# Kernel optimization log

Hardware: AMD Instinct MI355X
Metric: run time of the kernel (lower is better)

Reference implementation:

```python
import jax, jax.numpy as jnp
import numpy as np

B, S, HIDDEN = 8, 2048, 1024
NUM_GROUPS, NUM_VARS = 2, 320
CODEVECTOR_DIM = 256
TAU = 2.0  # module hardcodes self.temperature = 2
EPS_U = 1e-6


def setup_inputs() -> dict:
    key = jax.random.key(0)
    k1, k2, k3, k4 = jax.random.split(key, 4)
    hidden_states = jax.random.normal(k1, (B, S, HIDDEN), dtype=jnp.float32)
    W = jax.random.normal(k2, (NUM_GROUPS * NUM_VARS, HIDDEN), dtype=jnp.float32) * 0.02
    b = jnp.zeros((NUM_GROUPS * NUM_VARS,), dtype=jnp.float32)
    codevectors = jax.random.normal(
        k3, (1, NUM_GROUPS * NUM_VARS, CODEVECTOR_DIM // NUM_GROUPS), dtype=jnp.float32)
    gumbel_u = jax.random.uniform(
        k4, (B * S * NUM_GROUPS, NUM_VARS), minval=EPS_U, maxval=1.0 - EPS_U, dtype=jnp.float32)
    return {"hidden_states": hidden_states, "W": W, "b": b,
            "codevectors": codevectors, "gumbel_u": gumbel_u}


def reference(hidden_states, W, b, codevectors, gumbel_u):
    Bs, Ss, H = hidden_states.shape
    G, V = NUM_GROUPS, NUM_VARS
    N = Bs * Ss
    # weight_proj: [B,S,H] -> [B,S,G*V]
    logits = jnp.einsum('bsh,vh->bsv', hidden_states, W) + b
    logits = logits.reshape(N * G, V)
    # gumbel_softmax(tau=2, hard=True) -- training path
    gumbel = -jnp.log(-jnp.log(gumbel_u))
    y_soft = jax.nn.softmax((logits + gumbel) / TAU, axis=-1)
    idx = jnp.argmax(y_soft, axis=-1)
    y_hard = jax.nn.one_hot(idx, V, dtype=y_soft.dtype)
    # straight-through (hard value, soft gradient)
    codevector_probs = y_hard + y_soft - jax.lax.stop_gradient(y_soft)
    # perplexity over the soft (non-gumbel) distribution
    soft_dist = jax.nn.softmax(logits.reshape(N, G, V), axis=-1)
    marginal = soft_dist.mean(axis=0)                      # [G, V]
    perplexity = jnp.exp(-jnp.sum(marginal * jnp.log(marginal + 1e-7), axis=-1)).sum()
    # one-hot probs x codevectors, grouped sum: [N,G,V] x [G,V,d] -> [N,G,d]
    cv = codevectors.reshape(G, V, CODEVECTOR_DIM // G)
    out = jnp.einsum('ngv,gvd->ngd', codevector_probs.reshape(N, G, V), cv)
    out = out.reshape(Bs, Ss, CODEVECTOR_DIM)
    return out, perplexity
```

## Files before the change

### kernel.cpp

```cpp
#include <hip/hip_runtime.h>
#include <math.h>

#define NROWS 16384
#define HIDDEN 1024
#define NGROUPS 2
#define NVARS 320
#define NCOLS 640
#define CVDIM 256
#define OUT_ELEMS (NROWS * CVDIM)

#define BM 64
#define BK 32
#define NTHREADS 512
#define LGS 324

typedef __attribute__((ext_vector_type(8))) short short8;
typedef __attribute__((ext_vector_type(4))) float floatx4;

__device__ __forceinline__ ushort f32_to_bf16(float f) {
    unsigned u = __builtin_bit_cast(unsigned, f);
    unsigned r = (u + 0x7FFFu + ((u >> 16) & 1u)) >> 16;
    return (ushort)r;
}
__device__ __forceinline__ float bf16_to_f32(ushort u) {
    return __builtin_bit_cast(float, ((unsigned)u) << 16);
}

__global__ __launch_bounds__(256) void convert_bf16_kernel(
    const float* __restrict__ src, ushort* __restrict__ dst, int n8)
{
    const int i = blockIdx.x * 256 + threadIdx.x;
    if (i >= n8) return;
    const float4* s = reinterpret_cast<const float4*>(src) + (size_t)i * 2;
    const float4 v0 = s[0];
    const float4 v1 = s[1];
    uint4 p;
    p.x = (unsigned)f32_to_bf16(v0.x) | ((unsigned)f32_to_bf16(v0.y) << 16);
    p.y = (unsigned)f32_to_bf16(v0.z) | ((unsigned)f32_to_bf16(v0.w) << 16);
    p.z = (unsigned)f32_to_bf16(v1.x) | ((unsigned)f32_to_bf16(v1.y) << 16);
    p.w = (unsigned)f32_to_bf16(v1.z) | ((unsigned)f32_to_bf16(v1.w) << 16);
    reinterpret_cast<uint4*>(dst)[i] = p;
}

__device__ __forceinline__ void async16(const ushort* g, ushort* l) {
    __builtin_amdgcn_global_load_lds(
        (const __attribute__((address_space(1))) void*)g,
        (__attribute__((address_space(3))) void*)l,
        16, 0, 0);
}

__global__ __launch_bounds__(NTHREADS, 4) void fused_gvq_kernel(
    const float* __restrict__ X,
    const ushort* __restrict__ Wbf,
    const float* __restrict__ bias,
    const float* __restrict__ gu,
    const float* __restrict__ cv,
    float* __restrict__ out,
    float* __restrict__ marginal)
{
    __shared__ __align__(16) ushort lds[64 * LGS];
    ushort* As = lds;
    ushort* Bs = lds + 2048;

    const int tid = threadIdx.x;
    const int lane = tid & 63;
    const int w = tid >> 6;
    const int wm = w >> 2;
    const int wn = w & 3;
    const int mtile = blockIdx.x >> 1;
    const int g = blockIdx.x & 1;
    const int m0 = mtile * BM;
    const int n0 = g * NVARS;

    const int rm = lane & 15;
    const int kc = lane >> 4;

    floatx4 acc[2][5];
#pragma unroll
    for (int i = 0; i < 2; ++i)
#pragma unroll
        for (int j = 0; j < 5; ++j) acc[i][j] = (floatx4){0.f, 0.f, 0.f, 0.f};

    const int arow = tid >> 3;
    const int ak4 = (tid & 7) * 4;
    const float* Abase = X + (size_t)(m0 + arow) * HIDDEN + ak4;
    float4 areg = *reinterpret_cast<const float4*>(Abase);

    for (int k0 = 0; k0 < HIDDEN; k0 += BK) {
        uint2 pk;
        pk.x = (unsigned)f32_to_bf16(areg.x) | ((unsigned)f32_to_bf16(areg.y) << 16);
        pk.y = (unsigned)f32_to_bf16(areg.z) | ((unsigned)f32_to_bf16(areg.w) << 16);
        *reinterpret_cast<uint2*>(&As[arow * 32 + ak4]) = pk;
        {
            int c = tid;
            async16(Wbf + (size_t)(n0 + (c >> 2)) * HIDDEN + k0 + (c & 3) * 8, Bs + c * 8);
            c = tid + 512;
            async16(Wbf + (size_t)(n0 + (c >> 2)) * HIDDEN + k0 + (c & 3) * 8, Bs + c * 8);
            if (tid < 256) {
                c = tid + 1024;
                async16(Wbf + (size_t)(n0 + (c >> 2)) * HIDDEN + k0 + (c & 3) * 8, Bs + c * 8);
            }
        }
        __syncthreads();

        if (k0 + BK < HIDDEN)
            areg = *reinterpret_cast<const float4*>(Abase + k0 + BK);

        const short8* Asv = reinterpret_cast<const short8*>(As);
        const short8* Bsv = reinterpret_cast<const short8*>(Bs);
        short8 af[2], bf[5];
#pragma unroll
        for (int i = 0; i < 2; ++i)
            af[i] = Asv[(wm * 32 + i * 16 + rm) * 4 + kc];
#pragma unroll
        for (int j = 0; j < 5; ++j)
            bf[j] = Bsv[(wn * 80 + j * 16 + rm) * 4 + kc];
#pragma unroll
        for (int i = 0; i < 2; ++i)
#pragma unroll
            for (int j = 0; j < 5; ++j)
                acc[i][j] = __builtin_amdgcn_mfma_f32_16x16x32_bf16(
                    af[i], bf[j], acc[i][j], 0, 0, 0);
        __syncthreads();
    }

    const int cl = lane & 15;
    const int r4 = (lane >> 4) * 4;

    {
        float bj[5];
#pragma unroll
        for (int j = 0; j < 5; ++j) bj[j] = bias[n0 + wn * 80 + j * 16 + cl];
#pragma unroll
        for (int i = 0; i < 2; ++i)
#pragma unroll
            for (int j = 0; j < 5; ++j) {
                const int col = wn * 80 + j * 16 + cl;
#pragma unroll
                for (int q = 0; q < 4; ++q) {
                    const int lrow = wm * 32 + i * 16 + r4 + q;
                    lds[lrow * LGS + col] = f32_to_bf16(acc[i][j][q] + bj[j]);
                }
            }
    }
    __syncthreads();

    float macc[5];
#pragma unroll
    for (int j = 0; j < 5; ++j) macc[j] = 0.f;

    for (int s = 0; s < 8; ++s) {
        const int lrow = s * 8 + w;
        const int n = m0 + lrow;
        const size_t goff = ((size_t)n * 2 + g) * NVARS;

        float u5[5], lg[5];
#pragma unroll
        for (int j = 0; j < 5; ++j) u5[j] = gu[goff + lane + j * 64];
#pragma unroll
        for (int j = 0; j < 5; ++j) lg[j] = bf16_to_f32(lds[lrow * LGS + lane + j * 64]);

        float bk = lg[0] - __logf(-__logf(u5[0]));
        int bi = lane;
#pragma unroll
        for (int j = 1; j < 5; ++j) {
            const float kj = lg[j] - __logf(-__logf(u5[j]));
            const int v = lane + j * 64;
            if (kj > bk) { bk = kj; bi = v; }
        }
#pragma unroll
        for (int sh = 32; sh > 0; sh >>= 1) {
            const float ok = __shfl_xor(bk, sh);
            const int oi = __shfl_xor(bi, sh);
            if (ok > bk || (ok == bk && oi < bi)) { bk = ok; bi = oi; }
        }

        float p[5], sume = 0.f;
#pragma unroll
        for (int j = 0; j < 5; ++j) { p[j] = __expf(lg[j]); sume += p[j]; }
#pragma unroll
        for (int sh = 32; sh > 0; sh >>= 1) sume += __shfl_xor(sume, sh);
        const float inv = 1.f / sume;
#pragma unroll
        for (int j = 0; j < 5; ++j) macc[j] += p[j] * inv;

        const float2* cvrow =
            reinterpret_cast<const float2*>(cv + (size_t)(n0 + bi) * 128);
        reinterpret_cast<float2*>(out + (size_t)n * CVDIM + g * 128)[lane] = cvrow[lane];
    }

    __syncthreads();
    float* smr = reinterpret_cast<float*>(lds);
#pragma unroll
    for (int j = 0; j < 5; ++j) smr[w * NVARS + lane + j * 64] = macc[j];
    __syncthreads();
    if (tid < NVARS) {
        float sm = 0.f;
#pragma unroll
        for (int ww = 0; ww < 8; ++ww) sm += smr[ww * NVARS + tid];
        atomicAdd(&marginal[n0 + tid], sm);
    }
}

__global__ void perplexity_kernel(const float* __restrict__ marginal,
                                  float* __restrict__ out)
{
    const int lane = threadIdx.x;
    float h0 = 0.0f, h1 = 0.0f;
    for (int v = lane; v < NVARS; v += 64) {
        const float m0 = marginal[v] * (1.0f / (float)NROWS);
        h0 += m0 * logf(m0 + 1e-7f);
        const float m1 = marginal[NVARS + v] * (1.0f / (float)NROWS);
        h1 += m1 * logf(m1 + 1e-7f);
    }
#pragma unroll
    for (int s = 32; s > 0; s >>= 1) {
        h0 += __shfl_xor(h0, s);
        h1 += __shfl_xor(h1, s);
    }
    if (lane == 0) out[OUT_ELEMS] = expf(-h0) + expf(-h1);
}

extern "C" void kernel_launch(void* const* d_in, const int* in_sizes, int n_in,
                              void* d_out, int out_size, void* d_ws, size_t ws_size,
                              hipStream_t stream) {
    const float* X    = (const float*)d_in[0];
    const float* W    = (const float*)d_in[1];
    const float* bias = (const float*)d_in[2];
    const float* cv   = (const float*)d_in[3];
    const float* gu   = (const float*)d_in[4];
    float* out = (float*)d_out;

    ushort* Wbf      = (ushort*)d_ws;
    float*  marginal = (float*)(Wbf + (size_t)NCOLS * HIDDEN);

    hipMemsetAsync(marginal, 0, NCOLS * sizeof(float), stream);

    convert_bf16_kernel<<<(NCOLS * HIDDEN / 8 + 255) / 256, 256, 0, stream>>>(
        W, Wbf, NCOLS * HIDDEN / 8);

    fused_gvq_kernel<<<(NROWS / BM) * 2, NTHREADS, 0, stream>>>(
        X, Wbf, bias, gu, cv, out, marginal);

    perplexity_kernel<<<1, 64, 0, stream>>>(marginal, out);
}
```

Measured before the change: 69.26 us.

## Double-buffer GEMM LDS tiles and prefetch gumbel noise before epilogue sync

The K-loop now uses two LDS buffers for the A and B tiles. The next tile's bf16 A write and async B load are issued while MFMAs run on the current tile, and global A loads are prefetched two steps ahead. This removes one barrier per iteration and hides load latency behind compute. Gumbel uniforms for all eight epilogue rows are also loaded into registers before the post-GEMM barrier, so their latency overlaps the logits store. The trade is a larger LDS footprint and about 40 extra VGPRs per thread, which could limit occupancy or cause spills.

Measured after the change: 68.72 us. Within noise of the previous version (-0.8%).

```diff
diff --git a/kernel.cpp b/kernel.cpp
--- a/kernel.cpp
+++ b/kernel.cpp
@@ -3,7 +3,6 @@
 
 #define NROWS 16384
 #define HIDDEN 1024
-#define NGROUPS 2
 #define NVARS 320
 #define NCOLS 640
 #define CVDIM 256
@@ -13,14 +12,14 @@
 #define BK 32
 #define NTHREADS 512
 #define LGS 324
+#define BUFS 12288
 
 typedef __attribute__((ext_vector_type(8))) short short8;
 typedef __attribute__((ext_vector_type(4))) float floatx4;
 
-__device__ __forceinline__ ushort f32_to_bf16(float f) {
+__device__ __forceinline__ unsigned f32_to_bf16(float f) {
     unsigned u = __builtin_bit_cast(unsigned, f);
-    unsigned r = (u + 0x7FFFu + ((u >> 16) & 1u)) >> 16;
-    return (ushort)r;
+    return (u + 0x7FFFu + ((u >> 16) & 1u)) >> 16;
 }
 __device__ __forceinline__ float bf16_to_f32(ushort u) {
     return __builtin_bit_cast(float, ((unsigned)u) << 16);
@@ -35,10 +34,10 @@
     const float4 v0 = s[0];
     const float4 v1 = s[1];
     uint4 p;
-    p.x = (unsigned)f32_to_bf16(v0.x) | ((unsigned)f32_to_bf16(v0.y) << 16);
-    p.y = (unsigned)f32_to_bf16(v0.z) | ((unsigned)f32_to_bf16(v0.w) << 16);
-    p.z = (unsigned)f32_to_bf16(v1.x) | ((unsigned)f32_to_bf16(v1.y) << 16);
-    p.w = (unsigned)f32_to_bf16(v1.z) | ((unsigned)f32_to_bf16(v1.w) << 16);
+    p.x = f32_to_bf16(v0.x) | (f32_to_bf16(v0.y) << 16);
+    p.y = f32_to_bf16(v0.z) | (f32_to_bf16(v0.w) << 16);
+    p.z = f32_to_bf16(v1.x) | (f32_to_bf16(v1.y) << 16);
+    p.w = f32_to_bf16(v1.z) | (f32_to_bf16(v1.w) << 16);
     reinterpret_cast<uint4*>(dst)[i] = p;
 }
 
@@ -58,9 +57,7 @@
     float* __restrict__ out,
     float* __restrict__ marginal)
 {
-    __shared__ __align__(16) ushort lds[64 * LGS];
-    ushort* As = lds;
-    ushort* Bs = lds + 2048;
+    __shared__ __align__(16) ushort lds[2 * BUFS];
 
     const int tid = threadIdx.x;
     const int lane = tid & 63;
@@ -84,30 +81,50 @@
     const int arow = tid >> 3;
     const int ak4 = (tid & 7) * 4;
     const float* Abase = X + (size_t)(m0 + arow) * HIDDEN + ak4;
+
+#define WRITE_A(dstAs, v)                                                     \
+    {                                                                         \
+        uint2 pk;                                                             \
+        pk.x = f32_to_bf16((v).x) | (f32_to_bf16((v).y) << 16);               \
+        pk.y = f32_to_bf16((v).z) | (f32_to_bf16((v).w) << 16);               \
+        *reinterpret_cast<uint2*>(&(dstAs)[arow * 32 + ak4]) = pk;            \
+    }
+
+#define ISSUE_B(dstBs, kk)                                                    \
+    {                                                                         \
+        int c = tid;                                                          \
+        async16(Wbf + (size_t)(n0 + (c >> 2)) * HIDDEN + (kk) + (c & 3) * 8,  \
+                (dstBs) + c * 8);                                             \
+        c = tid + 512;                                                        \
+        async16(Wbf + (size_t)(n0 + (c >> 2)) * HIDDEN + (kk) + (c & 3) * 8,  \
+                (dstBs) + c * 8);                                             \
+        if (tid < 256) {                                                      \
+            c = tid + 1024;                                                   \
+            async16(Wbf + (size_t)(n0 + (c >> 2)) * HIDDEN + (kk) + (c & 3) * 8, \
+                    (dstBs) + c * 8);                                         \
+        }                                                                     \
+    }
+
     float4 areg = *reinterpret_cast<const float4*>(Abase);
-
-    for (int k0 = 0; k0 < HIDDEN; k0 += BK) {
-        uint2 pk;
-        pk.x = (unsigned)f32_to_bf16(areg.x) | ((unsigned)f32_to_bf16(areg.y) << 16);
-        pk.y = (unsigned)f32_to_bf16(areg.z) | ((unsigned)f32_to_bf16(areg.w) << 16);
-        *reinterpret_cast<uint2*>(&As[arow * 32 + ak4]) = pk;
-        {
-            int c = tid;
-            async16(Wbf + (size_t)(n0 + (c >> 2)) * HIDDEN + k0 + (c & 3) * 8, Bs + c * 8);
-            c = tid + 512;
-            async16(Wbf + (size_t)(n0 + (c >> 2)) * HIDDEN + k0 + (c & 3) * 8, Bs + c * 8);
-            if (tid < 256) {
-                c = tid + 1024;
-                async16(Wbf + (size_t)(n0 + (c >> 2)) * HIDDEN + k0 + (c & 3) * 8, Bs + c * 8);
-            }
+    WRITE_A(lds, areg);
+    ISSUE_B(lds + 2048, 0);
+    areg = *reinterpret_cast<const float4*>(Abase + BK);
+    __syncthreads();
+
+    for (int t = 0; t < 32; ++t) {
+        const int cur = t & 1;
+        ushort* base_c = lds + cur * BUFS;
+        ushort* base_n = lds + (cur ^ 1) * BUFS;
+
+        if (t < 31) {
+            WRITE_A(base_n, areg);
+            ISSUE_B(base_n + 2048, (t + 1) * BK);
         }
-        __syncthreads();
-
-        if (k0 + BK < HIDDEN)
-            areg = *reinterpret_cast<const float4*>(Abase + k0 + BK);
-
-        const short8* Asv = reinterpret_cast<const short8*>(As);
-        const short8* Bsv = reinterpret_cast<const short8*>(Bs);
+        if (t < 30)
+            areg = *reinterpret_cast<const float4*>(Abase + (t + 2) * BK);
+
+        const short8* Asv = reinterpret_cast<const short8*>(base_c);
+        const short8* Bsv = reinterpret_cast<const short8*>(base_c + 2048);
         short8 af[2], bf[5];
 #pragma unroll
         for (int i = 0; i < 2; ++i)
@@ -139,32 +156,40 @@
 #pragma unroll
                 for (int q = 0; q < 4; ++q) {
                     const int lrow = wm * 32 + i * 16 + r4 + q;
-                    lds[lrow * LGS + col] = f32_to_bf16(acc[i][j][q] + bj[j]);
+                    lds[lrow * LGS + col] = (ushort)f32_to_bf16(acc[i][j][q] + bj[j]);
                 }
             }
     }
+
+    float gup[8][5];
+#pragma unroll
+    for (int s = 0; s < 8; ++s) {
+        const int n = m0 + s * 8 + w;
+        const size_t goff = ((size_t)n * 2 + g) * NVARS + lane;
+#pragma unroll
+        for (int j = 0; j < 5; ++j) gup[s][j] = gu[goff + j * 64];
+    }
     __syncthreads();
 
     float macc[5];
 #pragma unroll
     for (int j = 0; j < 5; ++j) macc[j] = 0.f;
 
+#pragma unroll
     for (int s = 0; s < 8; ++s) {
         const int lrow = s * 8 + w;
         const int n = m0 + lrow;
-        const size_t goff = ((size_t)n * 2 + g) * NVARS;
-
-        float u5[5], lg[5];
-#pragma unroll
-        for (int j = 0; j < 5; ++j) u5[j] = gu[goff + lane + j * 64];
-#pragma unroll
-        for (int j = 0; j < 5; ++j) lg[j] = bf16_to_f32(lds[lrow * LGS + lane + j * 64]);
-
-        float bk = lg[0] - __logf(-__logf(u5[0]));
+
+        float lg[5];
+#pragma unroll
+        for (int j = 0; j < 5; ++j)
+            lg[j] = bf16_to_f32(lds[lrow * LGS + lane + j * 64]);
+
+        float bk = lg[0] - __logf(-__logf(gup[s][0]));
         int bi = lane;
 #pragma unroll
         for (int j = 1; j < 5; ++j) {
-            const float kj = lg[j] - __logf(-__logf(u5[j]));
+            const float kj = lg[j] - __logf(-__logf(gup[s][j]));
             const int v = lane + j * 64;
             if (kj > bk) { bk = kj; bi = v; }
         }
```

## Split fused kernel into tiled double-buffered GEMM and separate quantize pass

Applied to the files above, without the earlier changes.

Splits the fused GEMM+gumbel kernel in two. The first is a 128x128-tile bf16 MFMA GEMM with double-buffered LDS and register prefetch of X, writing bf16 logits to a workspace buffer. The second is a quantize kernel that reads those logits back for argmax, softmax and codevector gather. The goal is to stop each block re-reading X for its group, since the old grid converted X twice, and to improve MFMA reuse and occupancy. The cost is an extra global round-trip of 16384x640 bf16 logits and one more kernel launch.

Measured after the change: 95.44 us. 1.38x slower.

```diff
diff --git a/kernel.cpp b/kernel.cpp
--- a/kernel.cpp
+++ b/kernel.cpp
@@ -3,24 +3,17 @@
 
 #define NROWS 16384
 #define HIDDEN 1024
-#define NGROUPS 2
 #define NVARS 320
 #define NCOLS 640
 #define CVDIM 256
 #define OUT_ELEMS (NROWS * CVDIM)
 
-#define BM 64
-#define BK 32
-#define NTHREADS 512
-#define LGS 324
-
 typedef __attribute__((ext_vector_type(8))) short short8;
 typedef __attribute__((ext_vector_type(4))) float floatx4;
 
-__device__ __forceinline__ ushort f32_to_bf16(float f) {
+__device__ __forceinline__ unsigned f32_to_bf16(float f) {
     unsigned u = __builtin_bit_cast(unsigned, f);
-    unsigned r = (u + 0x7FFFu + ((u >> 16) & 1u)) >> 16;
-    return (ushort)r;
+    return (u + 0x7FFFu + ((u >> 16) & 1u)) >> 16;
 }
 __device__ __forceinline__ float bf16_to_f32(ushort u) {
     return __builtin_bit_cast(float, ((unsigned)u) << 16);
@@ -35,10 +28,10 @@
     const float4 v0 = s[0];
     const float4 v1 = s[1];
     uint4 p;
-    p.x = (unsigned)f32_to_bf16(v0.x) | ((unsigned)f32_to_bf16(v0.y) << 16);
-    p.y = (unsigned)f32_to_bf16(v0.z) | ((unsigned)f32_to_bf16(v0.w) << 16);
-    p.z = (unsigned)f32_to_bf16(v1.x) | ((unsigned)f32_to_bf16(v1.y) << 16);
-    p.w = (unsigned)f32_to_bf16(v1.z) | ((unsigned)f32_to_bf16(v1.w) << 16);
+    p.x = f32_to_bf16(v0.x) | (f32_to_bf16(v0.y) << 16);
+    p.y = f32_to_bf16(v0.z) | (f32_to_bf16(v0.w) << 16);
+    p.z = f32_to_bf16(v1.x) | (f32_to_bf16(v1.y) << 16);
+    p.w = f32_to_bf16(v1.z) | (f32_to_bf16(v1.w) << 16);
     reinterpret_cast<uint4*>(dst)[i] = p;
 }
 
@@ -49,116 +42,154 @@
         16, 0, 0);
 }
 
-__global__ __launch_bounds__(NTHREADS, 4) void fused_gvq_kernel(
+#define GBM 128
+#define GBN 128
+#define GBK 32
+
+__global__ __launch_bounds__(256, 3) void gemm_logits_kernel(
     const float* __restrict__ X,
     const ushort* __restrict__ Wbf,
     const float* __restrict__ bias,
+    ushort* __restrict__ Lg)
+{
+    __shared__ __align__(16) ushort lds[16384];
+
+    const int tid = threadIdx.x;
+    const int lane = tid & 63;
+    const int w = tid >> 6;
+    const int wm = w >> 1, wn = w & 1;
+
+    const int bid = blockIdx.x;
+    const int wg = (bid & 7) * 80 + (bid >> 3);
+    const int m0 = (wg / 5) * GBM;
+    const int n0 = (wg % 5) * GBN;
+
+    const int rm = lane & 15;
+    const int kc = lane >> 4;
+
+    floatx4 acc[4][4];
+#pragma unroll
+    for (int i = 0; i < 4; ++i)
+#pragma unroll
+        for (int j = 0; j < 4; ++j) acc[i][j] = (floatx4){0.f, 0.f, 0.f, 0.f};
+
+    const int arow = tid >> 1;
+    const int acol = (tid & 1) * 16;
+    const float* Aptr = X + (size_t)(m0 + arow) * HIDDEN + acol;
+
+    float4 a0, a1, a2, a3;
+#define LOAD_A(kk) { const float* p = Aptr + (kk);                             \
+    a0 = *(const float4*)(p);      a1 = *(const float4*)(p + 4);               \
+    a2 = *(const float4*)(p + 8);  a3 = *(const float4*)(p + 12); }
+
+#define WRITE_A(dst) { uint4 lo, hi;                                           \
+    lo.x = f32_to_bf16(a0.x) | (f32_to_bf16(a0.y) << 16);                      \
+    lo.y = f32_to_bf16(a0.z) | (f32_to_bf16(a0.w) << 16);                      \
+    lo.z = f32_to_bf16(a1.x) | (f32_to_bf16(a1.y) << 16);                      \
+    lo.w = f32_to_bf16(a1.z) | (f32_to_bf16(a1.w) << 16);                      \
+    hi.x = f32_to_bf16(a2.x) | (f32_to_bf16(a2.y) << 16);                      \
+    hi.y = f32_to_bf16(a2.z) | (f32_to_bf16(a2.w) << 16);                      \
+    hi.z = f32_to_bf16(a3.x) | (f32_to_bf16(a3.y) << 16);                      \
+    hi.w = f32_to_bf16(a3.z) | (f32_to_bf16(a3.w) << 16);                      \
+    uint4* d = (uint4*)((char*)(dst) + arow * 64 + acol * 2);                  \
+    d[0] = lo; d[1] = hi; }
+
+#define ISSUE_B(dst, kk) {                                                     \
+    int c = tid;                                                               \
+    async16(Wbf + (size_t)(n0 + (c >> 2)) * HIDDEN + (kk) + (c & 3) * 8,       \
+            (dst) + c * 8);                                                    \
+    c = tid + 256;                                                             \
+    async16(Wbf + (size_t)(n0 + (c >> 2)) * HIDDEN + (kk) + (c & 3) * 8,       \
+            (dst) + c * 8); }
+
+    LOAD_A(0);
+    WRITE_A(lds);
+    ISSUE_B(lds + 8192, 0);
+    LOAD_A(GBK);
+    __syncthreads();
+
+    for (int t = 0; t < 32; ++t) {
+        const int cur = t & 1;
+        ushort* Ac = lds + (cur ? 4096 : 0);
+        ushort* An = lds + (cur ? 0 : 4096);
+        ushort* Bc = lds + (cur ? 12288 : 8192);
+        ushort* Bn = lds + (cur ? 8192 : 12288);
+        if (t < 31) {
+            WRITE_A(An);
+            ISSUE_B(Bn, (t + 1) * GBK);
+        }
+        if (t < 30) LOAD_A((t + 2) * GBK);
+
+        const short8* Asv = reinterpret_cast<const short8*>(Ac);
+        const short8* Bsv = reinterpret_cast<const short8*>(Bc);
+        short8 af[4], bf[4];
+#pragma unroll
+        for (int f = 0; f < 4; ++f) {
+            af[f] = Asv[(wm * 64 + f * 16 + rm) * 4 + kc];
+            bf[f] = Bsv[(wn * 64 + f * 16 + rm) * 4 + kc];
+        }
+#pragma unroll
+        for (int i = 0; i < 4; ++i)
+#pragma unroll
+            for (int j = 0; j < 4; ++j)
+                acc[i][j] = __builtin_amdgcn_mfma_f32_16x16x32_bf16(
+                    af[i], bf[j], acc[i][j], 0, 0, 0);
+        __syncthreads();
+    }
+
+    const int cl = lane & 15;
+    const int r4 = (lane >> 4) * 4;
+    float bj[4];
+#pragma unroll
+    for (int j = 0; j < 4; ++j) bj[j] = bias[n0 + wn * 64 + j * 16 + cl];
+
+#pragma unroll
+    for (int i = 0; i < 4; ++i)
+#pragma unroll
+        for (int j = 0; j < 4; ++j) {
+            const int col = n0 + wn * 64 + j * 16 + cl;
+#pragma unroll
+            for (int q = 0; q < 4; ++q) {
+                const int row = m0 + wm * 64 + i * 16 + r4 + q;
+                unsigned v = f32_to_bf16(acc[i][j][q] + bj[j]);
+                unsigned o = (unsigned)__shfl_xor((int)v, 1);
+                if ((cl & 1) == 0)
+                    *reinterpret_cast<uint*>(Lg + (size_t)row * NCOLS + col) =
+                        v | (o << 16);
+            }
+        }
+}
+
+__global__ __launch_bounds__(256) void quantize_kernel(
+    const ushort* __restrict__ Lg,
     const float* __restrict__ gu,
     const float* __restrict__ cv,
     float* __restrict__ out,
     float* __restrict__ marginal)
 {
-    __shared__ __align__(16) ushort lds[64 * LGS];
-    ushort* As = lds;
-    ushort* Bs = lds + 2048;
-
+    __shared__ float smr[4][NVARS];
     const int tid = threadIdx.x;
+    const int w = tid >> 6;
     const int lane = tid & 63;
-    const int w = tid >> 6;
-    const int wm = w >> 2;
-    const int wn = w & 3;
-    const int mtile = blockIdx.x >> 1;
-    const int g = blockIdx.x & 1;
-    const int m0 = mtile * BM;
-    const int n0 = g * NVARS;
-
-    const int rm = lane & 15;
-    const int kc = lane >> 4;
-
-    floatx4 acc[2][5];
-#pragma unroll
-    for (int i = 0; i < 2; ++i)
-#pragma unroll
-        for (int j = 0; j < 5; ++j) acc[i][j] = (floatx4){0.f, 0.f, 0.f, 0.f};
-
-    const int arow = tid >> 3;
-    const int ak4 = (tid & 7) * 4;
-    const float* Abase = X + (size_t)(m0 + arow) * HIDDEN + ak4;
-    float4 areg = *reinterpret_cast<const float4*>(Abase);
-
-    for (int k0 = 0; k0 < HIDDEN; k0 += BK) {
-        uint2 pk;
-        pk.x = (unsigned)f32_to_bf16(areg.x) | ((unsigned)f32_to_bf16(areg.y) << 16);
-        pk.y = (unsigned)f32_to_bf16(areg.z) | ((unsigned)f32_to_bf16(areg.w) << 16);
-        *reinterpret_cast<uint2*>(&As[arow * 32 + ak4]) = pk;
-        {
-            int c = tid;
-            async16(Wbf + (size_t)(n0 + (c >> 2)) * HIDDEN + k0 + (c & 3) * 8, Bs + c * 8);
-            c = tid + 512;
-            async16(Wbf + (size_t)(n0 + (c >> 2)) * HIDDEN + k0 + (c & 3) * 8, Bs + c * 8);
-            if (tid < 256) {
-                c = tid + 1024;
-                async16(Wbf + (size_t)(n0 + (c >> 2)) * HIDDEN + k0 + (c & 3) * 8, Bs + c * 8);
-            }
-        }
-        __syncthreads();
-
-        if (k0 + BK < HIDDEN)
-            areg = *reinterpret_cast<const float4*>(Abase + k0 + BK);
-
-        const short8* Asv = reinterpret_cast<const short8*>(As);
-        const short8* Bsv = reinterpret_cast<const short8*>(Bs);
-        short8 af[2], bf[5];
-#pragma unroll
-        for (int i = 0; i < 2; ++i)
-            af[i] = Asv[(wm * 32 + i * 16 + rm) * 4 + kc];
-#pragma unroll
-        for (int j = 0; j < 5; ++j)
-            bf[j] = Bsv[(wn * 80 + j * 16 + rm) * 4 + kc];
-#pragma unroll
-        for (int i = 0; i < 2; ++i)
-#pragma unroll
-            for (int j = 0; j < 5; ++j)
-                acc[i][j] = __builtin_amdgcn_mfma_f32_16x16x32_bf16(
-                    af[i], bf[j], acc[i][j], 0, 0, 0);
-        __syncthreads();
-    }
-
-    const int cl = lane & 15;
-    const int r4 = (lane >> 4) * 4;
-
-    {
-        float bj[5];
-#pragma unroll
-        for (int j = 0; j < 5; ++j) bj[j] = bias[n0 + wn * 80 + j * 16 + cl];
-#pragma unroll
-        for (int i = 0; i < 2; ++i)
-#pragma unroll
-            for (int j = 0; j < 5; ++j) {
-                const int col = wn * 80 + j * 16 + cl;
-#pragma unroll
-                for (int q = 0; q < 4; ++q) {
-                    const int lrow = wm * 32 + i * 16 + r4 + q;
-                    lds[lrow * LGS + col] = f32_to_bf16(acc[i][j][q] + bj[j]);
-                }
-            }
-    }
-    __syncthreads();
 
     float macc[5];
 #pragma unroll
     for (int j = 0; j < 5; ++j) macc[j] = 0.f;
 
-    for (int s = 0; s < 8; ++s) {
-        const int lrow = s * 8 + w;
-        const int n = m0 + lrow;
-        const size_t goff = ((size_t)n * 2 + g) * NVARS;
-
-        float u5[5], lg[5];
+    const int g = w & 1;
+
+#pragma unroll
+    for (int t = 0; t < 8; ++t) {
+        const int r = blockIdx.x * 32 + t * 4 + w;
+        const int n = r >> 1;
+        const size_t loff = (size_t)n * NCOLS + g * NVARS;
+        const size_t goff = (size_t)r * NVARS;
+
+        float lg[5], u5[5];
 #pragma unroll
         for (int j = 0; j < 5; ++j) u5[j] = gu[goff + lane + j * 64];
 #pragma unroll
-        for (int j = 0; j < 5; ++j) lg[j] = bf16_to_f32(lds[lrow * LGS + lane + j * 64]);
+        for (int j = 0; j < 5; ++j) lg[j] = bf16_to_f32(Lg[loff + lane + j * 64]);
 
         float bk = lg[0] - __logf(-__logf(u5[0]));
         int bi = lane;
@@ -185,20 +216,16 @@
         for (int j = 0; j < 5; ++j) macc[j] += p[j] * inv;
 
         const float2* cvrow =
-            reinterpret_cast<const float2*>(cv + (size_t)(n0 + bi) * 128);
+            reinterpret_cast<const float2*>(cv + (size_t)(g * NVARS + bi) * 128);
         reinterpret_cast<float2*>(out + (size_t)n * CVDIM + g * 128)[lane] = cvrow[lane];
     }
 
+#pragma unroll
+    for (int j = 0; j < 5; ++j) smr[w][lane + j * 64] = macc[j];
     __syncthreads();
-    float* smr = reinterpret_cast<float*>(lds);
-#pragma unroll
-    for (int j = 0; j < 5; ++j) smr[w * NVARS + lane + j * 64] = macc[j];
-    __syncthreads();
-    if (tid < NVARS) {
-        float sm = 0.f;
-#pragma unroll
-        for (int ww = 0; ww < 8; ++ww) sm += smr[ww * NVARS + tid];
-        atomicAdd(&marginal[n0 + tid], sm);
+    for (int i = tid; i < NVARS; i += 256) {
+        atomicAdd(&marginal[i], smr[0][i] + smr[2][i]);
+        atomicAdd(&marginal[NVARS + i], smr[1][i] + smr[3][i]);
     }
 }
 
@@ -232,15 +259,19 @@
     float* out = (float*)d_out;
 
     ushort* Wbf      = (ushort*)d_ws;
-    float*  marginal = (float*)(Wbf + (size_t)NCOLS * HIDDEN);
-
-    hipMemsetAsync(marginal, 0, NCOLS * sizeof(float), stream);
+    ushort* Lg       = Wbf + (size_t)NCOLS * HIDDEN;
+    float*  marginal = (float*)(Lg + (size_t)NROWS * NCOLS);
+
+    (void)hipMemsetAsync(marginal, 0, NCOLS * sizeof(float), stream);
 
     convert_bf16_kernel<<<(NCOLS * HIDDEN / 8 + 255) / 256, 256, 0, stream>>>(
         W, Wbf, NCOLS * HIDDEN / 8);
 
-    fused_gvq_kernel<<<(NROWS / BM) * 2, NTHREADS, 0, stream>>>(
-        X, Wbf, bias, gu, cv, out, marginal);
+    gemm_logits_kernel<<<(NROWS / GBM) * (NCOLS / GBN), 256, 0, stream>>>(
+        X, Wbf, bias, Lg);
+
+    quantize_kernel<<<(NROWS * 2) / 32, 256, 0, stream>>>(
+        Lg, gu, cv, out, marginal);
 
     perplexity_kernel<<<1, 64, 0, stream>>>(marginal, out);
 }
```
